# Kernel optimization log

Measured on AMD Instinct MI355X. Metric: run time of the kernel, lower is better.

Reference implementation:

```python
import jax, jax.numpy as jnp
import numpy as np

B, L, E, H = 4, 2048, 1024, 16
D = E // H  # head_dim = 64

def setup_inputs() -> dict:
    key = jax.random.key(0)
    ks = jax.random.split(key, 8)
    s = 1.0 / np.sqrt(E)
    return {
        "x_q": jax.random.normal(ks[0], (B, L, E), jnp.float32),
        "x_k": jax.random.normal(ks[1], (B, L, E), jnp.float32),
        "x_v": jax.random.normal(ks[2], (B, L, E), jnp.float32),
        "Wq": jax.random.uniform(ks[3], (E, E), jnp.float32, -s, s),
        "Wk": jax.random.uniform(ks[4], (E, E), jnp.float32, -s, s),
        "Wv": jax.random.uniform(ks[5], (E, E), jnp.float32, -s, s),
        "Wo": jax.random.uniform(ks[6], (E, E), jnp.float32, -s, s),
        "bo": jax.random.uniform(ks[7], (E,), jnp.float32, -s, s),
    }

def reference(x_q, x_k, x_v, Wq, Wk, Wv, Wo, bo):
    # projections (torch Linear: y = x @ W.T)
    Q = (x_q @ Wq.T).reshape(B, L, H, D).transpose(0, 2, 1, 3)  # (B,H,Lq,D)
    K = (x_k @ Wk.T).reshape(B, L, H, D).transpose(0, 2, 1, 3)
    V = (x_v @ Wv.T).reshape(B, L, H, D).transpose(0, 2, 1, 3)
    scale = 1.0 / jnp.sqrt(jnp.asarray(D, Q.dtype))
    scores = jnp.einsum('bhqd,bhkd->bhqk', Q, K) * scale  # (B,H,Lq,Lk)
    attn = jax.nn.softmax(scores, axis=-1)
    ctx = jnp.einsum('bhqk,bhkd->bhqd', attn, V)
    ctx = ctx.transpose(0, 2, 1, 3).reshape(B, L, E)
    return ctx @ Wo.T + bo
```

## Files before the change

kernel.cpp:

```cpp
#include <hip/hip_runtime.h>
#include <hip/hip_bf16.h>
#include <stdint.h>

typedef __bf16 bf16;
typedef __attribute__((ext_vector_type(8))) __bf16 bf16x8;
typedef __attribute__((ext_vector_type(4))) __bf16 bf16x4;
typedef __attribute__((ext_vector_type(4))) float f32x4;
typedef __attribute__((ext_vector_type(16))) float f32x16;
typedef __attribute__((ext_vector_type(4))) unsigned int u32x4;

#define MFMA(a, b, c) __builtin_amdgcn_mfma_f32_16x16x32_bf16(a, b, c, 0, 0, 0)
#define MFMA32(a, b, c) __builtin_amdgcn_mfma_f32_32x32x16_bf16(a, b, c, 0, 0, 0)

__device__ __forceinline__ void gload16(const void* g, void* l) {
  __builtin_amdgcn_global_load_lds(
      (const __attribute__((address_space(1))) void*)g,
      (__attribute__((address_space(3))) void*)l, 16, 0, 0);
}

__global__ void cvt4(const float* __restrict__ s0, const float* __restrict__ s1,
                     const float* __restrict__ s2, const float* __restrict__ s3,
                     bf16* __restrict__ d0, bf16* __restrict__ d1,
                     bf16* __restrict__ d2, bf16* __restrict__ d3, long n) {
  const float* s = blockIdx.y == 0 ? s0 : blockIdx.y == 1 ? s1 : blockIdx.y == 2 ? s2 : s3;
  bf16* d       = blockIdx.y == 0 ? d0 : blockIdx.y == 1 ? d1 : blockIdx.y == 2 ? d2 : d3;
  long i0 = ((long)blockIdx.x * blockDim.x + threadIdx.x) * 8;
  long gs = (long)gridDim.x * blockDim.x * 8;
  for (long i = i0; i < n; i += gs) {
    float4 a = *(const float4*)(s + i);
    float4 b = *(const float4*)(s + i + 4);
    bf16x8 ov;
    ov[0] = (bf16)a.x; ov[1] = (bf16)a.y; ov[2] = (bf16)a.z; ov[3] = (bf16)a.w;
    ov[4] = (bf16)b.x; ov[5] = (bf16)b.y; ov[6] = (bf16)b.z; ov[7] = (bf16)b.w;
    *(bf16x8*)(d + i) = ov;
  }
}

__global__ __launch_bounds__(256) void gemm_bt(const bf16* __restrict__ A,
                                               const bf16* __restrict__ W,
                                               void* __restrict__ Cout,
                                               const float* __restrict__ bias,
                                               float scale, int mode) {
  __shared__ bf16 As[128 * 64];
  __shared__ bf16 Bs[128 * 64];
  const int tid = threadIdx.x;
  const int l = tid & 63, w = tid >> 6;
  const int lr = l & 15, lg = l >> 4;
  const int lin = blockIdx.y * 8 + blockIdx.x;
  const int nl = (lin & 7) * 64 + (lin >> 3);
  const int m0 = (nl >> 3) * 128, n0 = (nl & 7) * 128;
  const int wm = w >> 1, wn = w & 1;
  f32x4 acc[4][4];
  for (int i = 0; i < 4; i++)
    for (int j = 0; j < 4; j++)
      for (int r = 0; r < 4; r++) acc[i][j][r] = 0.f;

  const int srow = tid >> 3;
  const int schunk = tid & 7;

  for (int kt = 0; kt < 1024; kt += 64) {
#pragma unroll
    for (int i = 0; i < 4; i++) {
      int ar = i * 32 + srow;
      int ac = schunk ^ (ar & 7);
      gload16(A + (long)(m0 + ar) * 1024 + kt + ac * 8, (char*)As + i * 4096 + tid * 16);
      gload16(W + (long)(n0 + ar) * 1024 + kt + ac * 8, (char*)Bs + i * 4096 + tid * 16);
    }
    __syncthreads();
#pragma unroll
    for (int h = 0; h < 2; h++) {
      bf16x8 af[4], bw[4];
#pragma unroll
      for (int i = 0; i < 4; i++) {
        int row = wm * 64 + i * 16 + lr;
        af[i] = *(const bf16x8*)((const char*)As + row * 128 + (((h * 4 + lg) ^ (lr & 7)) << 4));
      }
#pragma unroll
      for (int j = 0; j < 4; j++) {
        int row = wn * 64 + j * 16 + lr;
        bw[j] = *(const bf16x8*)((const char*)Bs + row * 128 + (((h * 4 + lg) ^ (lr & 7)) << 4));
      }
#pragma unroll
      for (int i = 0; i < 4; i++)
#pragma unroll
        for (int j = 0; j < 4; j++)
          acc[i][j] = MFMA(af[i], bw[j], acc[i][j]);
    }
    __syncthreads();
  }

  for (int i = 0; i < 4; i++)
    for (int j = 0; j < 4; j++) {
      int row = m0 + wm * 64 + i * 16 + lg * 4;
      int col = n0 + wn * 64 + j * 16 + lr;
      f32x4 v = acc[i][j];
      if (mode == 2) {
        float* O = (float*)Cout;
        float bb = bias[col];
        for (int r = 0; r < 4; r++) O[(long)(row + r) * 1024 + col] = v[r] + bb;
      } else if (mode == 0) {
        bf16* O = (bf16*)Cout;
        for (int r = 0; r < 4; r++) {
          int rr = row + r;
          long idx = ((long)((rr >> 11) * 16 + (col >> 6)) * 2048 + (rr & 2047)) * 64 + (col & 63);
          O[idx] = (bf16)(v[r] * scale);
        }
      } else {
        bf16* O = (bf16*)Cout;
        long idx = ((long)((row >> 11) * 16 + (col >> 6)) * 64 + (col & 63)) * 2048 + (row & 2047);
        bf16x4 pk;
        for (int r = 0; r < 4; r++) pk[r] = (bf16)v[r];
        *(bf16x4*)(O + idx) = pk;
      }
    }
}

__global__ __launch_bounds__(512, 4) void attn_fwd(const bf16* __restrict__ Q,
                                                   const bf16* __restrict__ K,
                                                   const bf16* __restrict__ Vt,
                                                   bf16* __restrict__ ctx) {
  __shared__ bf16 Ks[2][128 * 64];
  __shared__ bf16 Vs[2][64 * 128];
  const int tid = threadIdx.x;
  const int l = tid & 63, w = tid >> 6;
  const int q32 = l & 31, hl = l >> 5;
  const int lin = blockIdx.y * 8 + blockIdx.x;
  const int nl = (lin & 7) * 64 + (lin >> 3);
  const int bh = nl >> 3, qt = nl & 7;
  const bf16* Qh = Q + (long)bh * 2048 * 64;
  const bf16* Kh = K + (long)bh * 2048 * 64;
  const bf16* Vh = Vt + (long)bh * 64 * 2048;
  const int qb = qt * 256 + w * 32;

#define STAGE(kv0, buf)                                                          \
  {                                                                              \
    _Pragma("unroll") for (int i = 0; i < 2; i++) {                              \
      int c = i * 512 + tid;                                                     \
      int kr = c >> 3, kc = c & 7;                                               \
      gload16(Kh + (long)((kv0) + kr) * 64 + ((kc ^ (kr & 7)) << 3),             \
              (char*)Ks[buf] + c * 16);                                          \
    }                                                                            \
    _Pragma("unroll") for (int i = 0; i < 2; i++) {                              \
      int c = i * 512 + tid;                                                     \
      int vr = c >> 4, vc = c & 15;                                              \
      int vsw = (vc & 8) | ((vc & 7) ^ (vr & 7));                                \
      gload16(Vh + (long)vr * 2048 + (kv0) + vsw * 8,                            \
              (char*)Vs[buf] + c * 16);                                          \
    }                                                                            \
  }

  bf16x8 bq[4];
#pragma unroll
  for (int kk = 0; kk < 4; kk++)
    bq[kk] = *(const bf16x8*)(Qh + (long)(qb + q32) * 64 + kk * 16 + hl * 8);

  f32x16 o0, o1;
#pragma unroll
  for (int r = 0; r < 16; r++) { o0[r] = 0.f; o1[r] = 0.f; }
  float lrun = 0.f;

  STAGE(0, 0);
  __syncthreads();

  for (int t = 0; t < 16; t++) {
    const int cur = t & 1;
    if (t < 15) STAGE((t + 1) * 128, cur ^ 1);
    const bf16* Kc = Ks[cur];
    const bf16* Vc = Vs[cur];
    f32x4 psum = {0.f, 0.f, 0.f, 0.f};

#pragma unroll
    for (int nn = 0; nn < 4; nn++) {
      const int row = nn * 32 + q32;
      f32x16 acc;
#pragma unroll
      for (int r = 0; r < 16; r++) acc[r] = 0.f;
      __builtin_amdgcn_s_setprio(1);
#pragma unroll
      for (int kk = 0; kk < 4; kk++) {
        int ch = (kk * 2 + hl) ^ (row & 7);
        bf16x8 ak = *(const bf16x8*)((const char*)Kc + row * 128 + (ch << 4));
        acc = MFMA32(ak, bq[kk], acc);
      }
      __builtin_amdgcn_s_setprio(0);

      f32x16 p;
#pragma unroll
      for (int r = 0; r < 16; r++) p[r] = __builtin_amdgcn_exp2f(acc[r]);
      f32x4 t4;
#pragma unroll
      for (int j = 0; j < 4; j++) t4[j] = (p[j] + p[4 + j]) + (p[8 + j] + p[12 + j]);
      psum += t4;

      unsigned wd[8];
#pragma unroll
      for (int i = 0; i < 8; i++) {
        float lo = p[2 * i], hi = p[2 * i + 1];
        asm("v_cvt_pk_bf16_f32 %0, %1, %2" : "=v"(wd[i]) : "v"(lo), "v"(hi));
      }
#pragma unroll
      for (int ss = 0; ss < 2; ss++) {
        unsigned a0 = wd[ss * 4 + 0], b0 = wd[ss * 4 + 2];
        unsigned a1 = wd[ss * 4 + 1], b1 = wd[ss * 4 + 3];
        asm("v_permlane32_swap_b32 %0, %1" : "+v"(a0), "+v"(b0));
        asm("v_permlane32_swap_b32 %0, %1" : "+v"(a1), "+v"(b1));
        u32x4 pw = {a0, a1, b0, b1};
        bf16x8 bp = *(bf16x8*)&pw;
        int ch0 = (nn * 2 + ss) * 2 + hl;
        __builtin_amdgcn_s_setprio(1);
#pragma unroll
        for (int nd = 0; nd < 2; nd++) {
          int vrw = nd * 32 + q32;
          int ch = (ch0 & 8) | ((ch0 & 7) ^ (vrw & 7));
          bf16x8 av = *(const bf16x8*)((const char*)Vc + vrw * 256 + (ch << 4));
          if (nd == 0) o0 = MFMA32(av, bp, o0);
          else         o1 = MFMA32(av, bp, o1);
        }
        __builtin_amdgcn_s_setprio(0);
      }
    }
    lrun += (psum[0] + psum[1]) + (psum[2] + psum[3]);
    __syncthreads();
  }

  lrun += __shfl_xor(lrun, 32);
  const int b = bh >> 4, h = bh & 15;
  const float inv = 1.0f / lrun;
  const int q = qb + q32;
#pragma unroll
  for (int nd = 0; nd < 2; nd++)
#pragma unroll
    for (int qd = 0; qd < 4; qd++) {
      bf16x4 pk;
#pragma unroll
      for (int r = 0; r < 4; r++)
        pk[r] = (bf16)((nd == 0 ? o0[qd * 4 + r] : o1[qd * 4 + r]) * inv);
      int d = nd * 32 + qd * 8 + hl * 4;
      *(bf16x4*)(ctx + ((long)b * 2048 + q) * 1024 + h * 64 + d) = pk;
    }
#undef STAGE
}

extern "C" void kernel_launch(void* const* d_in, const int* in_sizes, int n_in,
                              void* d_out, int out_size, void* d_ws, size_t ws_size,
                              hipStream_t stream) {
  const float* xq = (const float*)d_in[0];
  const float* xk = (const float*)d_in[1];
  const float* xv = (const float*)d_in[2];
  const float* Wq = (const float*)d_in[3];
  const float* Wk = (const float*)d_in[4];
  const float* Wv = (const float*)d_in[5];
  const float* Wo = (const float*)d_in[6];
  const float* bo = (const float*)d_in[7];

  char* p = (char*)d_ws;
  const size_t SZ_X = (size_t)8192 * 1024 * 2;
  const size_t SZ_W = (size_t)1024 * 1024 * 2;
  bf16* xqb = (bf16*)p; p += SZ_X;
  bf16* xkb = (bf16*)p; p += SZ_X;
  bf16* xvb = (bf16*)p; p += SZ_X;
  bf16* wqb = (bf16*)p; p += SZ_W;
  bf16* wkb = (bf16*)p; p += SZ_W;
  bf16* wvb = (bf16*)p; p += SZ_W;
  bf16* wob = (bf16*)p; p += SZ_W;
  bf16* Qb  = (bf16*)p; p += SZ_X;
  bf16* Kb  = (bf16*)p; p += SZ_X;
  bf16* Vtb = (bf16*)p; p += SZ_X;
  bf16* ctxb = (bf16*)p; p += SZ_X;
  (void)ws_size; (void)in_sizes; (void)n_in; (void)out_size;

  const float QSCALE = 0.18033688011112042f;

  cvt4<<<dim3(1024, 3), 256, 0, stream>>>(xq, xk, xv, xq, xqb, xkb, xvb, xqb,
                                          (long)8192 * 1024);
  cvt4<<<dim3(128, 4), 256, 0, stream>>>(Wq, Wk, Wv, Wo, wqb, wkb, wvb, wob,
                                         (long)1024 * 1024);
  gemm_bt<<<dim3(8, 64), 256, 0, stream>>>(xqb, wqb, Qb, nullptr, QSCALE, 0);
  gemm_bt<<<dim3(8, 64), 256, 0, stream>>>(xkb, wkb, Kb, nullptr, 1.0f, 0);
  gemm_bt<<<dim3(8, 64), 256, 0, stream>>>(xvb, wvb, Vtb, nullptr, 1.0f, 1);
  attn_fwd<<<dim3(8, 64), 512, 0, stream>>>(Qb, Kb, Vtb, ctxb);
  gemm_bt<<<dim3(8, 64), 256, 0, stream>>>(ctxb, wob, d_out, bo, 1.0f, 2);
}
```

Measured before the change: 205.0 us.

## Double-buffer GEMM staging, batch QKV projections, shrink attention KV tile

The GEMM main loop now double-buffers the A/W shared tiles, so the next K-slice loads are issued while the current slice runs through MFMA. The three Q/K/V projection launches are merged into one launch with a z-dimension, which relies on the bf16 input, weight and output buffers sitting contiguously in the workspace. The attention kernel halves its KV tile to 64 rows with a simpler swizzle and raises launch bounds to 8 waves-per-EU to increase occupancy, at the cost of twice as many barriers per key sweep.

```diff
diff --git a/kernel.cpp b/kernel.cpp
--- a/kernel.cpp
+++ b/kernel.cpp
@@ -36,13 +36,12 @@
   }
 }
 
-__global__ __launch_bounds__(256) void gemm_bt(const bf16* __restrict__ A,
-                                               const bf16* __restrict__ W,
-                                               void* __restrict__ Cout,
-                                               const float* __restrict__ bias,
-                                               float scale, int mode) {
-  __shared__ bf16 As[128 * 64];
-  __shared__ bf16 Bs[128 * 64];
+__device__ __forceinline__ void gemm_body(const bf16* __restrict__ A,
+                                          const bf16* __restrict__ W,
+                                          void* __restrict__ Cout,
+                                          const float* __restrict__ bias,
+                                          float scale, int mode,
+                                          bf16* As, bf16* Bs) {
   const int tid = threadIdx.x;
   const int l = tid & 63, w = tid >> 6;
   const int lr = l & 15, lg = l >> 4;
@@ -58,27 +57,38 @@
   const int srow = tid >> 3;
   const int schunk = tid & 7;
 
-  for (int kt = 0; kt < 1024; kt += 64) {
-#pragma unroll
-    for (int i = 0; i < 4; i++) {
-      int ar = i * 32 + srow;
-      int ac = schunk ^ (ar & 7);
-      gload16(A + (long)(m0 + ar) * 1024 + kt + ac * 8, (char*)As + i * 4096 + tid * 16);
-      gload16(W + (long)(n0 + ar) * 1024 + kt + ac * 8, (char*)Bs + i * 4096 + tid * 16);
-    }
-    __syncthreads();
+#define GSTAGE(kt, buf)                                                          \
+  {                                                                              \
+    _Pragma("unroll") for (int i = 0; i < 4; i++) {                              \
+      int ar = i * 32 + srow;                                                    \
+      int ac = schunk ^ (ar & 7);                                                \
+      gload16(A + (long)(m0 + ar) * 1024 + (kt) + ac * 8,                        \
+              (char*)As + (buf) * 16384 + i * 4096 + tid * 16);                  \
+      gload16(W + (long)(n0 + ar) * 1024 + (kt) + ac * 8,                        \
+              (char*)Bs + (buf) * 16384 + i * 4096 + tid * 16);                  \
+    }                                                                            \
+  }
+
+  GSTAGE(0, 0);
+  __syncthreads();
+
+  for (int t = 0; t < 16; t++) {
+    const int cur = t & 1;
+    if (t < 15) GSTAGE((t + 1) * 64, cur ^ 1);
+    const char* Ac = (const char*)As + cur * 16384;
+    const char* Bc = (const char*)Bs + cur * 16384;
 #pragma unroll
     for (int h = 0; h < 2; h++) {
       bf16x8 af[4], bw[4];
 #pragma unroll
       for (int i = 0; i < 4; i++) {
         int row = wm * 64 + i * 16 + lr;
-        af[i] = *(const bf16x8*)((const char*)As + row * 128 + (((h * 4 + lg) ^ (lr & 7)) << 4));
+        af[i] = *(const bf16x8*)(Ac + row * 128 + (((h * 4 + lg) ^ (lr & 7)) << 4));
       }
 #pragma unroll
       for (int j = 0; j < 4; j++) {
         int row = wn * 64 + j * 16 + lr;
-        bw[j] = *(const bf16x8*)((const char*)Bs + row * 128 + (((h * 4 + lg) ^ (lr & 7)) << 4));
+        bw[j] = *(const bf16x8*)(Bc + row * 128 + (((h * 4 + lg) ^ (lr & 7)) << 4));
       }
 #pragma unroll
       for (int i = 0; i < 4; i++)
@@ -88,6 +98,7 @@
     }
     __syncthreads();
   }
+#undef GSTAGE
 
   for (int i = 0; i < 4; i++)
     for (int j = 0; j < 4; j++) {
@@ -115,12 +126,36 @@
     }
 }
 
-__global__ __launch_bounds__(512, 4) void attn_fwd(const bf16* __restrict__ Q,
+__global__ __launch_bounds__(256) void gemm_qkv(const bf16* __restrict__ Xb,
+                                                const bf16* __restrict__ Wb,
+                                                bf16* __restrict__ Ob,
+                                                float qscale) {
+  __shared__ bf16 As[2][128 * 64];
+  __shared__ bf16 Bs[2][128 * 64];
+  const int z = blockIdx.z;
+  const bf16* A = Xb + (long)z * 8192 * 1024;
+  const bf16* W = Wb + (long)z * 1024 * 1024;
+  bf16* O = Ob + (long)z * 8192 * 1024;
+  const float scale = (z == 0) ? qscale : 1.0f;
+  const int mode = (z == 2) ? 1 : 0;
+  gemm_body(A, W, O, nullptr, scale, mode, &As[0][0], &Bs[0][0]);
+}
+
+__global__ __launch_bounds__(256) void gemm_out(const bf16* __restrict__ A,
+                                                const bf16* __restrict__ W,
+                                                float* __restrict__ Cout,
+                                                const float* __restrict__ bias) {
+  __shared__ bf16 As[2][128 * 64];
+  __shared__ bf16 Bs[2][128 * 64];
+  gemm_body(A, W, Cout, bias, 1.0f, 2, &As[0][0], &Bs[0][0]);
+}
+
+__global__ __launch_bounds__(512, 8) void attn_fwd(const bf16* __restrict__ Q,
                                                    const bf16* __restrict__ K,
                                                    const bf16* __restrict__ Vt,
                                                    bf16* __restrict__ ctx) {
-  __shared__ bf16 Ks[2][128 * 64];
-  __shared__ bf16 Vs[2][64 * 128];
+  __shared__ bf16 Ks[2][64 * 64];
+  __shared__ bf16 Vs[2][64 * 64];
   const int tid = threadIdx.x;
   const int l = tid & 63, w = tid >> 6;
   const int q32 = l & 31, hl = l >> 5;
@@ -132,21 +167,14 @@
   const bf16* Vh = Vt + (long)bh * 64 * 2048;
   const int qb = qt * 256 + w * 32;
 
+  const int sr = tid >> 3, sc = tid & 7;
+
 #define STAGE(kv0, buf)                                                          \
   {                                                                              \
-    _Pragma("unroll") for (int i = 0; i < 2; i++) {                              \
-      int c = i * 512 + tid;                                                     \
-      int kr = c >> 3, kc = c & 7;                                               \
-      gload16(Kh + (long)((kv0) + kr) * 64 + ((kc ^ (kr & 7)) << 3),             \
-              (char*)Ks[buf] + c * 16);                                          \
-    }                                                                            \
-    _Pragma("unroll") for (int i = 0; i < 2; i++) {                              \
-      int c = i * 512 + tid;                                                     \
-      int vr = c >> 4, vc = c & 15;                                              \
-      int vsw = (vc & 8) | ((vc & 7) ^ (vr & 7));                                \
-      gload16(Vh + (long)vr * 2048 + (kv0) + vsw * 8,                            \
-              (char*)Vs[buf] + c * 16);                                          \
-    }                                                                            \
+    gload16(Kh + (long)((kv0) + sr) * 64 + ((sc ^ (sr & 7)) << 3),               \
+            (char*)Ks[buf] + tid * 16);                                          \
+    gload16(Vh + (long)sr * 2048 + (kv0) + ((sc ^ (sr & 7)) << 3),               \
+            (char*)Vs[buf] + tid * 16);                                          \
   }
 
   bf16x8 bq[4];
@@ -162,15 +190,15 @@
   STAGE(0, 0);
   __syncthreads();
 
-  for (int t = 0; t < 16; t++) {
+  for (int t = 0; t < 32; t++) {
     const int cur = t & 1;
-    if (t < 15) STAGE((t + 1) * 128, cur ^ 1);
+    if (t < 31) STAGE((t + 1) * 64, cur ^ 1);
     const bf16* Kc = Ks[cur];
     const bf16* Vc = Vs[cur];
     f32x4 psum = {0.f, 0.f, 0.f, 0.f};
 
 #pragma unroll
-    for (int nn = 0; nn < 4; nn++) {
+    for (int nn = 0; nn < 2; nn++) {
       const int row = nn * 32 + q32;
       f32x16 acc;
 #pragma unroll
@@ -178,7 +206,7 @@
       __builtin_amdgcn_s_setprio(1);
 #pragma unroll
       for (int kk = 0; kk < 4; kk++) {
-        int ch = (kk * 2 + hl) ^ (row & 7);
+        int ch = (kk * 2 + hl) ^ (q32 & 7);
         bf16x8 ak = *(const bf16x8*)((const char*)Kc + row * 128 + (ch << 4));
         acc = MFMA32(ak, bq[kk], acc);
       }
@@ -211,8 +239,8 @@
 #pragma unroll
         for (int nd = 0; nd < 2; nd++) {
           int vrw = nd * 32 + q32;
-          int ch = (ch0 & 8) | ((ch0 & 7) ^ (vrw & 7));
-          bf16x8 av = *(const bf16x8*)((const char*)Vc + vrw * 256 + (ch << 4));
+          int ch = ch0 ^ (q32 & 7);
+          bf16x8 av = *(const bf16x8*)((const char*)Vc + vrw * 128 + (ch << 4));
           if (nd == 0) o0 = MFMA32(av, bp, o0);
           else         o1 = MFMA32(av, bp, o1);
         }
@@ -275,9 +303,7 @@
                                           (long)8192 * 1024);
   cvt4<<<dim3(128, 4), 256, 0, stream>>>(Wq, Wk, Wv, Wo, wqb, wkb, wvb, wob,
                                          (long)1024 * 1024);
-  gemm_bt<<<dim3(8, 64), 256, 0, stream>>>(xqb, wqb, Qb, nullptr, QSCALE, 0);
-  gemm_bt<<<dim3(8, 64), 256, 0, stream>>>(xkb, wkb, Kb, nullptr, 1.0f, 0);
-  gemm_bt<<<dim3(8, 64), 256, 0, stream>>>(xvb, wvb, Vtb, nullptr, 1.0f, 1);
+  gemm_qkv<<<dim3(8, 64, 3), 256, 0, stream>>>(xqb, wqb, Qb, QSCALE);
   attn_fwd<<<dim3(8, 64), 512, 0, stream>>>(Qb, Kb, Vtb, ctxb);
-  gemm_bt<<<dim3(8, 64), 256, 0, stream>>>(ctxb, wob, d_out, bo, 1.0f, 2);
-}
+  gemm_out<<<dim3(8, 64), 256, 0, stream>>>(ctxb, wob, (float*)d_out, bo);
+}
```

Measured after the change: 515.2 us. 2.51x slower.
